# Kernel optimization log

Measured on AMD Instinct MI355X. Metric: run time of the kernel, lower is better.

Reference implementation:

```python
import jax, jax.numpy as jnp
import numpy as np

W_DIM = 512   # latent dim
CH = 512      # number of Fourier channels / output channels
SIZE = 64     # spatial size (square: size[0]=size[1])
SR = 64.0     # sampling_rate
BW = 2.0      # bandwidth
BATCH = 32


def setup_inputs() -> dict:
    key = jax.random.key(0)
    k1, k2, k3, k4, k5 = jax.random.split(key, 5)
    w = jax.random.normal(k1, (BATCH, W_DIM), jnp.float32)
    # affine FC params (weight_init=0 in original; use small random so t varies)
    affine_w = jax.random.normal(k2, (4, W_DIM), jnp.float32) * 0.1
    affine_b = jnp.array([1.0, 0.0, 0.0, 0.0], jnp.float32)
    # channel-mixing weight
    weight = jax.random.normal(k3, (CH, CH), jnp.float32)
    # freqs buffer init: randn, normalized by r*exp(r^2/4), scaled by bandwidth
    f = jax.random.normal(k4, (CH, 2), jnp.float32)
    radii = jnp.sqrt(jnp.sum(f * f, axis=1, keepdims=True))
    f = f / (radii * jnp.exp(radii * radii / 4.0)) * BW
    phases = jax.random.uniform(k5, (CH,), jnp.float32) - 0.5
    return {"w": w, "affine_w": affine_w, "affine_b": affine_b,
            "weight": weight, "freqs": f, "phases": phases}


def reference(w, affine_w, affine_b, weight, freqs, phases):
    # affine FC: FullyConnectedLayer with lr_multiplier=1 -> weight_gain = 1/sqrt(in)
    gain = np.float32(1.0 / np.sqrt(W_DIM))
    t = w @ (affine_w.T * gain) + affine_b                      # [N, 4]
    t = t / jnp.linalg.norm(t[:, :2], axis=1, keepdims=True)
    c, s, tx, ty = t[:, 0], t[:, 1], t[:, 2], t[:, 3]
    # combined transform = m_r @ m_t @ I; top-left 2x2 rotation block:
    R = jnp.stack([jnp.stack([c, -s], -1),
                   jnp.stack([s, c], -1)], axis=1)              # [N, 2, 2]
    # translation column of combined transform (m_r @ m_t)[:, :2, 2]
    trans = jnp.stack([-c * tx + s * ty, -s * tx - c * ty], -1) # [N, 2]
    ph = phases[None, :] + jnp.einsum('cd,nd->nc', freqs, trans)  # [N, C]
    fr = jnp.einsum('cd,nde->nce', freqs, R)                      # [N, C, 2]
    amp = jnp.clip(1.0 - (jnp.linalg.norm(fr, axis=2) - BW) / (SR / 2.0 - BW), 0.0, 1.0)  # [N, C]
    # affine_grid(theta, [1,1,H,W], align_corners=False): base coords (2i+1)/D - 1
    scale = np.float32(0.5 * SIZE / SR)
    xs = ((2.0 * jnp.arange(SIZE, dtype=jnp.float32) + 1.0) / SIZE - 1.0) * scale
    ys = ((2.0 * jnp.arange(SIZE, dtype=jnp.float32) + 1.0) / SIZE - 1.0) * scale
    grid = jnp.stack([jnp.broadcast_to(xs[None, :], (SIZE, SIZE)),
                      jnp.broadcast_to(ys[:, None], (SIZE, SIZE))], axis=-1)  # [H, W, 2]
    # per-pixel Fourier phase: [N, H, W, C]
    x = jnp.einsum('hwd,ncd->nhwc', grid, fr) + ph[:, None, None, :]
    x = jnp.sin(x * np.float32(2.0 * np.pi)) * amp[:, None, None, :]
    # channel projection, then to NCHW
    x = jnp.einsum('nhwc,kc->nkhw', x, weight * np.float32(1.0 / np.sqrt(CH)))
    return x  # [N, CH, H, W]
```

## Files before the change

kernel.cpp:

```cpp
#include <hip/hip_runtime.h>
#include <hip/hip_bf16.h>

#define WDIM 512
#define CHN  512
#define NB   32
#define SZ   64
#define MTOT 4096

typedef __attribute__((ext_vector_type(4))) float f32x4;
typedef __attribute__((ext_vector_type(8))) short short8;
typedef __attribute__((ext_vector_type(4))) int   int4v;
typedef __attribute__((ext_vector_type(4))) float float4v;

__global__ __launch_bounds__(512) void setup_kernel(
    const float* __restrict__ w,
    const float* __restrict__ affine_w,
    const float* __restrict__ affine_b,
    const float* __restrict__ freqs,
    const float* __restrict__ phases,
    float* __restrict__ frx_o, float* __restrict__ fry_o,
    float* __restrict__ pha_o, float* __restrict__ amp_o)
{
    const int n = blockIdx.x;
    const int tid = threadIdx.x;
    __shared__ float red[8][4];
    __shared__ float par[4];

    float wv = w[n * WDIM + tid];
    float p0 = wv * affine_w[0 * WDIM + tid];
    float p1 = wv * affine_w[1 * WDIM + tid];
    float p2 = wv * affine_w[2 * WDIM + tid];
    float p3 = wv * affine_w[3 * WDIM + tid];
    #pragma unroll
    for (int off = 32; off >= 1; off >>= 1) {
        p0 += __shfl_down(p0, off);
        p1 += __shfl_down(p1, off);
        p2 += __shfl_down(p2, off);
        p3 += __shfl_down(p3, off);
    }
    const int wave = tid >> 6;
    if ((tid & 63) == 0) {
        red[wave][0] = p0; red[wave][1] = p1;
        red[wave][2] = p2; red[wave][3] = p3;
    }
    __syncthreads();
    if (tid == 0) {
        const float gain = 0.04419417382415922f;
        float t[4];
        #pragma unroll
        for (int j = 0; j < 4; ++j) {
            float s = 0.0f;
            #pragma unroll
            for (int v = 0; v < 8; ++v) s += red[v][j];
            t[j] = s * gain + affine_b[j];
        }
        float inv = 1.0f / sqrtf(t[0] * t[0] + t[1] * t[1]);
        float c = t[0] * inv, s = t[1] * inv, tx = t[2] * inv, ty = t[3] * inv;
        par[0] = c;
        par[1] = s;
        par[2] = -c * tx + s * ty;
        par[3] = -s * tx - c * ty;
    }
    __syncthreads();
    const float c_ = par[0], s_ = par[1], tr0 = par[2], tr1 = par[3];
    const int ci = tid;
    float fx = freqs[ci * 2 + 0], fy = freqs[ci * 2 + 1];
    float frx = fx * c_ + fy * s_;
    float fry = -fx * s_ + fy * c_;
    float ph = phases[ci] + fx * tr0 + fy * tr1;
    float r = sqrtf(frx * frx + fry * fry);
    float amp = 1.0f - (r - 2.0f) * (1.0f / 30.0f);
    amp = fminf(fmaxf(amp, 0.0f), 1.0f);
    frx_o[n * CHN + ci] = frx;
    fry_o[n * CHN + ci] = fry;
    pha_o[n * CHN + ci] = ph;
    amp_o[n * CHN + ci] = amp;
}

__global__ __launch_bounds__(512) void prep_kernel(
    const float* __restrict__ frx, const float* __restrict__ amp,
    const float* __restrict__ wsrc,
    float* __restrict__ SA, float* __restrict__ CA,
    __hip_bfloat16* __restrict__ wbf)
{
    const int b = blockIdx.x;
    if (b < NB * 64) {
        const int n = b >> 6;
        const int w = b & 63;
        const int c = threadIdx.x;
        float f = frx[n * CHN + c];
        float a = amp[n * CHN + c];
        float xs = (float)(2 * w + 1) * (1.0f / 128.0f) - 0.5f;
        float arg = xs * f;
        size_t idx = ((size_t)(n * 64 + w)) * CHN + c;
        SA[idx] = a * __builtin_amdgcn_sinf(arg);
        CA[idx] = a * __builtin_amdgcn_cosf(arg);
    } else {
        int i = (b - NB * 64) * 512 + threadIdx.x;
        wbf[i] = __float2bfloat16(wsrc[i] * 0.04419417382415922f);
    }
}

__global__ __launch_bounds__(256, 2) void fused_kernel(
    const float* __restrict__ fry, const float* __restrict__ pha,
    const float* __restrict__ SA, const float* __restrict__ CA,
    const __hip_bfloat16* __restrict__ wbf,
    float* __restrict__ out)
{
    __shared__ __align__(16) __hip_bfloat16 As[128 * 64];
    __shared__ __align__(16) __hip_bfloat16 Bs[256 * 64];
    __shared__ __align__(16) float sB[2][CHN];
    __shared__ __align__(16) float cB[2][CHN];

    const int tid = threadIdx.x;
    const int mb = blockIdx.x * 128;
    const int kb = blockIdx.y * 256;
    const int n  = blockIdx.z;
    const int h0 = mb >> 6;

    #pragma unroll
    for (int u = 0; u < 2; ++u) {
        int c = tid + u * 256;
        float fy = fry[n * CHN + c];
        float ph = pha[n * CHN + c];
        #pragma unroll
        for (int hh = 0; hh < 2; ++hh) {
            float ys = (float)(2 * (h0 + hh) + 1) * (1.0f / 128.0f) - 0.5f;
            float bv = ys * fy + ph;
            sB[hh][c] = __builtin_amdgcn_sinf(bv);
            cB[hh][c] = __builtin_amdgcn_cosf(bv);
        }
    }

    const int lane = tid & 63;
    const int wid  = tid >> 6;
    const int ln15 = lane & 15;
    const int hi4  = lane >> 4;
    const int wk   = wid * 64;

    const int cc0 = (tid & 7) * 8;
    const int rb  = tid >> 3;

    const float* saL = SA + ((size_t)(n * 64 + rb)) * CHN + cc0;
    const float* saH = saL + 32 * CHN;
    const float* caL = CA + ((size_t)(n * 64 + rb)) * CHN + cc0;
    const float* caH = caL + 32 * CHN;

    f32x4 acc[4][8];
    #pragma unroll
    for (int a = 0; a < 4; ++a)
        #pragma unroll
        for (int b = 0; b < 8; ++b)
            acc[a][b] = (f32x4)0.0f;

    #pragma unroll 1
    for (int kc = 0; kc < 8; ++kc) {
        const int c0 = kc * 64;
        __syncthreads();

        #pragma unroll
        for (int u = 0; u < 8; ++u) {
            int unit = u * 256 + tid;
            int row = unit >> 3;
            int cbyte = ((unit & 7) << 4) ^ ((row & 7) << 4);
            const __hip_bfloat16* src = wbf + (size_t)(kb + row) * CHN + c0 + (cbyte >> 1);
            char* ldsbase = (char*)Bs + (u * 256 + (wid << 6)) * 16;
            __builtin_amdgcn_global_load_lds(
                (const __attribute__((address_space(1))) unsigned int*)src,
                (__attribute__((address_space(3))) unsigned int*)ldsbase, 16, 0, 0);
        }

        float4v s0 = *(const float4v*)(saL + c0), s1 = *(const float4v*)(saL + c0 + 4);
        float4v s2 = *(const float4v*)(saH + c0), s3 = *(const float4v*)(saH + c0 + 4);
        float4v q0 = *(const float4v*)(caL + c0), q1 = *(const float4v*)(caL + c0 + 4);
        float4v q2 = *(const float4v*)(caH + c0), q3 = *(const float4v*)(caH + c0 + 4);
        #pragma unroll
        for (int i = 0; i < 4; ++i) {
            int m = rb + i * 32;
            int hh = i >> 1;
            float4v A0 = (i & 1) ? s2 : s0, A1 = (i & 1) ? s3 : s1;
            float4v C0 = (i & 1) ? q2 : q0, C1 = (i & 1) ? q3 : q1;
            float4v B0 = *(const float4v*)&sB[hh][c0 + cc0];
            float4v B1 = *(const float4v*)&sB[hh][c0 + cc0 + 4];
            float4v D0 = *(const float4v*)&cB[hh][c0 + cc0];
            float4v D1 = *(const float4v*)&cB[hh][c0 + cc0 + 4];
            union { __hip_bfloat16 h[8]; int4v v; } t;
            #pragma unroll
            for (int j = 0; j < 4; ++j)
                t.h[j] = __float2bfloat16(A0[j] * D0[j] + C0[j] * B0[j]);
            #pragma unroll
            for (int j = 0; j < 4; ++j)
                t.h[4 + j] = __float2bfloat16(A1[j] * D1[j] + C1[j] * B1[j]);
            *(int4v*)((char*)As + m * 128 + ((cc0 * 2) ^ ((m & 7) << 4))) = t.v;
        }
        __syncthreads();

        #pragma unroll
        for (int kk = 0; kk < 2; ++kk) {
            short8 wf[4], ff[8];
            #pragma unroll
            for (int ki = 0; ki < 4; ++ki) {
                int row = wk + ki * 16 + ln15;
                wf[ki] = *(const short8*)((char*)Bs + row * 128 +
                          (((kk * 32 + hi4 * 8) * 2) ^ ((row & 7) << 4)));
            }
            #pragma unroll
            for (int mj = 0; mj < 8; ++mj) {
                int m = mj * 16 + ln15;
                ff[mj] = *(const short8*)((char*)As + m * 128 +
                          (((kk * 32 + hi4 * 8) * 2) ^ ((m & 7) << 4)));
            }
            #pragma unroll
            for (int ki = 0; ki < 4; ++ki)
                #pragma unroll
                for (int mj = 0; mj < 8; ++mj)
                    acc[ki][mj] = __builtin_amdgcn_mfma_f32_16x16x32_bf16(
                        wf[ki], ff[mj], acc[ki][mj], 0, 0, 0);
        }
    }

    #pragma unroll
    for (int ki = 0; ki < 4; ++ki) {
        #pragma unroll
        for (int mj = 0; mj < 8; ++mj) {
            int kg = kb + wk + ki * 16 + hi4 * 4;
            int mg = mb + mj * 16 + ln15;
            float* op = out + ((size_t)n * CHN + kg) * MTOT + mg;
            #pragma unroll
            for (int r = 0; r < 4; ++r)
                op[(size_t)r * MTOT] = acc[ki][mj][r];
        }
    }
}

extern "C" void kernel_launch(void* const* d_in, const int* in_sizes, int n_in,
                              void* d_out, int out_size, void* d_ws, size_t ws_size,
                              hipStream_t stream) {
    const float* w        = (const float*)d_in[0];
    const float* affine_w = (const float*)d_in[1];
    const float* affine_b = (const float*)d_in[2];
    const float* weight   = (const float*)d_in[3];
    const float* freqs    = (const float*)d_in[4];
    const float* phases   = (const float*)d_in[5];
    float* out = (float*)d_out;

    char* ws = (char*)d_ws;
    float* frx = (float*)(ws + 0);
    float* fry = (float*)(ws + 65536);
    float* pha = (float*)(ws + 131072);
    float* amp = (float*)(ws + 196608);
    __hip_bfloat16* wbf = (__hip_bfloat16*)(ws + 262144);
    float* SA = (float*)(ws + 786432);
    float* CA = (float*)(ws + 786432 + 4194304);

    setup_kernel<<<NB, 512, 0, stream>>>(w, affine_w, affine_b, freqs, phases,
                                         frx, fry, pha, amp);
    prep_kernel<<<NB * 64 + (CHN * CHN) / 512, 512, 0, stream>>>(
        frx, amp, weight, SA, CA, wbf);

    dim3 grid(MTOT / 128, CHN / 256, NB);
    fused_kernel<<<grid, 256, 0, stream>>>(fry, pha, SA, CA, wbf, out);
}
```

Before: 112.7 us.

## Double-buffer weight tiles and precompute row sin/cos tables in prep kernel

The fused GEMM kernel now double-buffers the bf16 weight tile in LDS. It issues the next chunk's global-to-LDS loads and A-operand loads before running MFMAs on the current chunk, using custom barriers with explicit waitcnt. The per-row sin/cos tables are moved out of the fused kernel into prep_kernel and written to global memory, so the fused kernel no longer spends time on transcendentals at its start. This adds LDS use (an extra 32KB buffer), which may limit occupancy, and adds extra global traffic for the SB/CB tables.

```diff
diff --git a/kernel.cpp b/kernel.cpp
--- a/kernel.cpp
+++ b/kernel.cpp
@@ -11,6 +11,20 @@
 typedef __attribute__((ext_vector_type(8))) short short8;
 typedef __attribute__((ext_vector_type(4))) int   int4v;
 typedef __attribute__((ext_vector_type(4))) float float4v;
+
+#define SBAR() __builtin_amdgcn_sched_barrier(0)
+__device__ __forceinline__ void bar_lgkm() {
+    SBAR();
+    asm volatile("s_waitcnt lgkmcnt(0)" ::: "memory");
+    __builtin_amdgcn_s_barrier();
+    SBAR();
+}
+__device__ __forceinline__ void bar_full() {
+    SBAR();
+    asm volatile("s_waitcnt vmcnt(0) lgkmcnt(0)" ::: "memory");
+    __builtin_amdgcn_s_barrier();
+    SBAR();
+}
 
 __global__ __launch_bounds__(512) void setup_kernel(
     const float* __restrict__ w,
@@ -78,9 +92,11 @@
 }
 
 __global__ __launch_bounds__(512) void prep_kernel(
-    const float* __restrict__ frx, const float* __restrict__ amp,
+    const float* __restrict__ frx, const float* __restrict__ fry,
+    const float* __restrict__ pha, const float* __restrict__ amp,
     const float* __restrict__ wsrc,
     float* __restrict__ SA, float* __restrict__ CA,
+    float* __restrict__ SB, float* __restrict__ CB,
     __hip_bfloat16* __restrict__ wbf)
 {
     const int b = blockIdx.x;
@@ -88,13 +104,17 @@
         const int n = b >> 6;
         const int w = b & 63;
         const int c = threadIdx.x;
-        float f = frx[n * CHN + c];
-        float a = amp[n * CHN + c];
+        float fx = frx[n * CHN + c];
+        float a  = amp[n * CHN + c];
+        float fy = fry[n * CHN + c];
+        float ph = pha[n * CHN + c];
         float xs = (float)(2 * w + 1) * (1.0f / 128.0f) - 0.5f;
-        float arg = xs * f;
         size_t idx = ((size_t)(n * 64 + w)) * CHN + c;
-        SA[idx] = a * __builtin_amdgcn_sinf(arg);
-        CA[idx] = a * __builtin_amdgcn_cosf(arg);
+        SA[idx] = a * __builtin_amdgcn_sinf(xs * fx);
+        CA[idx] = a * __builtin_amdgcn_cosf(xs * fx);
+        float bb = xs * fy + ph;
+        SB[idx] = __builtin_amdgcn_sinf(bb);
+        CB[idx] = __builtin_amdgcn_cosf(bb);
     } else {
         int i = (b - NB * 64) * 512 + threadIdx.x;
         wbf[i] = __float2bfloat16(wsrc[i] * 0.04419417382415922f);
@@ -102,15 +122,13 @@
 }
 
 __global__ __launch_bounds__(256, 2) void fused_kernel(
-    const float* __restrict__ fry, const float* __restrict__ pha,
     const float* __restrict__ SA, const float* __restrict__ CA,
+    const float* __restrict__ SB, const float* __restrict__ CB,
     const __hip_bfloat16* __restrict__ wbf,
     float* __restrict__ out)
 {
     __shared__ __align__(16) __hip_bfloat16 As[128 * 64];
-    __shared__ __align__(16) __hip_bfloat16 Bs[256 * 64];
-    __shared__ __align__(16) float sB[2][CHN];
-    __shared__ __align__(16) float cB[2][CHN];
+    __shared__ __align__(16) __hip_bfloat16 Bs[2][256 * 64];
 
     const int tid = threadIdx.x;
     const int mb = blockIdx.x * 128;
@@ -118,20 +136,6 @@
     const int n  = blockIdx.z;
     const int h0 = mb >> 6;
 
-    #pragma unroll
-    for (int u = 0; u < 2; ++u) {
-        int c = tid + u * 256;
-        float fy = fry[n * CHN + c];
-        float ph = pha[n * CHN + c];
-        #pragma unroll
-        for (int hh = 0; hh < 2; ++hh) {
-            float ys = (float)(2 * (h0 + hh) + 1) * (1.0f / 128.0f) - 0.5f;
-            float bv = ys * fy + ph;
-            sB[hh][c] = __builtin_amdgcn_sinf(bv);
-            cB[hh][c] = __builtin_amdgcn_cosf(bv);
-        }
-    }
-
     const int lane = tid & 63;
     const int wid  = tid >> 6;
     const int ln15 = lane & 15;
@@ -145,63 +149,69 @@
     const float* saH = saL + 32 * CHN;
     const float* caL = CA + ((size_t)(n * 64 + rb)) * CHN + cc0;
     const float* caH = caL + 32 * CHN;
-
-    f32x4 acc[4][8];
-    #pragma unroll
-    for (int a = 0; a < 4; ++a)
-        #pragma unroll
-        for (int b = 0; b < 8; ++b)
-            acc[a][b] = (f32x4)0.0f;
-
-    #pragma unroll 1
-    for (int kc = 0; kc < 8; ++kc) {
-        const int c0 = kc * 64;
-        __syncthreads();
-
+    const float* sb0 = SB + ((size_t)(n * 64 + h0)) * CHN + cc0;
+    const float* cb0 = CB + ((size_t)(n * 64 + h0)) * CHN + cc0;
+
+    auto stageB = [&](int buf, int c0) {
         #pragma unroll
         for (int u = 0; u < 8; ++u) {
             int unit = u * 256 + tid;
             int row = unit >> 3;
             int cbyte = ((unit & 7) << 4) ^ ((row & 7) << 4);
             const __hip_bfloat16* src = wbf + (size_t)(kb + row) * CHN + c0 + (cbyte >> 1);
-            char* ldsbase = (char*)Bs + (u * 256 + (wid << 6)) * 16;
+            char* ldsbase = (char*)Bs[buf] + (u * 256 + (wid << 6)) * 16;
             __builtin_amdgcn_global_load_lds(
                 (const __attribute__((address_space(1))) unsigned int*)src,
                 (__attribute__((address_space(3))) unsigned int*)ldsbase, 16, 0, 0);
         }
-
-        float4v s0 = *(const float4v*)(saL + c0), s1 = *(const float4v*)(saL + c0 + 4);
-        float4v s2 = *(const float4v*)(saH + c0), s3 = *(const float4v*)(saH + c0 + 4);
-        float4v q0 = *(const float4v*)(caL + c0), q1 = *(const float4v*)(caL + c0 + 4);
-        float4v q2 = *(const float4v*)(caH + c0), q3 = *(const float4v*)(caH + c0 + 4);
+    };
+
+    float4v Ps0, Ps1, Ps2, Ps3, Pq0, Pq1, Pq2, Pq3;
+    auto loadP = [&](int c0) {
+        Ps0 = *(const float4v*)(saL + c0); Ps1 = *(const float4v*)(saL + c0 + 4);
+        Ps2 = *(const float4v*)(saH + c0); Ps3 = *(const float4v*)(saH + c0 + 4);
+        Pq0 = *(const float4v*)(caL + c0); Pq1 = *(const float4v*)(caL + c0 + 4);
+        Pq2 = *(const float4v*)(caH + c0); Pq3 = *(const float4v*)(caH + c0 + 4);
+    };
+
+    auto features = [&](int c0) {
+        float4v B00 = *(const float4v*)(sb0 + c0),       B01 = *(const float4v*)(sb0 + c0 + 4);
+        float4v B10 = *(const float4v*)(sb0 + CHN + c0), B11 = *(const float4v*)(sb0 + CHN + c0 + 4);
+        float4v D00 = *(const float4v*)(cb0 + c0),       D01 = *(const float4v*)(cb0 + c0 + 4);
+        float4v D10 = *(const float4v*)(cb0 + CHN + c0), D11 = *(const float4v*)(cb0 + CHN + c0 + 4);
         #pragma unroll
         for (int i = 0; i < 4; ++i) {
             int m = rb + i * 32;
-            int hh = i >> 1;
-            float4v A0 = (i & 1) ? s2 : s0, A1 = (i & 1) ? s3 : s1;
-            float4v C0 = (i & 1) ? q2 : q0, C1 = (i & 1) ? q3 : q1;
-            float4v B0 = *(const float4v*)&sB[hh][c0 + cc0];
-            float4v B1 = *(const float4v*)&sB[hh][c0 + cc0 + 4];
-            float4v D0 = *(const float4v*)&cB[hh][c0 + cc0];
-            float4v D1 = *(const float4v*)&cB[hh][c0 + cc0 + 4];
+            float4v A0 = (i & 1) ? Ps2 : Ps0, A1 = (i & 1) ? Ps3 : Ps1;
+            float4v C0 = (i & 1) ? Pq2 : Pq0, C1 = (i & 1) ? Pq3 : Pq1;
+            float4v Sb0 = (i >> 1) ? B10 : B00, Sb1 = (i >> 1) ? B11 : B01;
+            float4v Cb0 = (i >> 1) ? D10 : D00, Cb1 = (i >> 1) ? D11 : D01;
             union { __hip_bfloat16 h[8]; int4v v; } t;
             #pragma unroll
             for (int j = 0; j < 4; ++j)
-                t.h[j] = __float2bfloat16(A0[j] * D0[j] + C0[j] * B0[j]);
+                t.h[j] = __float2bfloat16(A0[j] * Cb0[j] + C0[j] * Sb0[j]);
             #pragma unroll
             for (int j = 0; j < 4; ++j)
-                t.h[4 + j] = __float2bfloat16(A1[j] * D1[j] + C1[j] * B1[j]);
+                t.h[4 + j] = __float2bfloat16(A1[j] * Cb1[j] + C1[j] * Sb1[j]);
             *(int4v*)((char*)As + m * 128 + ((cc0 * 2) ^ ((m & 7) << 4))) = t.v;
         }
-        __syncthreads();
-
+    };
+
+    f32x4 acc[4][8];
+    #pragma unroll
+    for (int a = 0; a < 4; ++a)
+        #pragma unroll
+        for (int b = 0; b < 8; ++b)
+            acc[a][b] = (f32x4)0.0f;
+
+    auto mfmaStep = [&](int buf) {
         #pragma unroll
         for (int kk = 0; kk < 2; ++kk) {
             short8 wf[4], ff[8];
             #pragma unroll
             for (int ki = 0; ki < 4; ++ki) {
                 int row = wk + ki * 16 + ln15;
-                wf[ki] = *(const short8*)((char*)Bs + row * 128 +
+                wf[ki] = *(const short8*)((char*)Bs[buf] + row * 128 +
                           (((kk * 32 + hi4 * 8) * 2) ^ ((row & 7) << 4)));
             }
             #pragma unroll
@@ -217,7 +227,24 @@
                     acc[ki][mj] = __builtin_amdgcn_mfma_f32_16x16x32_bf16(
                         wf[ki], ff[mj], acc[ki][mj], 0, 0, 0);
         }
-    }
+    };
+
+    stageB(0, 0);
+    loadP(0);
+    features(0);
+    bar_full();
+
+    #pragma unroll 1
+    for (int kc = 0; kc < 7; ++kc) {
+        const int c0n = (kc + 1) * 64;
+        stageB((kc + 1) & 1, c0n);
+        loadP(c0n);
+        mfmaStep(kc & 1);
+        bar_lgkm();
+        features(c0n);
+        bar_full();
+    }
+    mfmaStep(1);
 
     #pragma unroll
     for (int ki = 0; ki < 4; ++ki) {
@@ -250,14 +277,16 @@
     float* pha = (float*)(ws + 131072);
     float* amp = (float*)(ws + 196608);
     __hip_bfloat16* wbf = (__hip_bfloat16*)(ws + 262144);
-    float* SA = (float*)(ws + 786432);
-    float* CA = (float*)(ws + 786432 + 4194304);
+    float* SA = (float*)(ws + (1u << 20));
+    float* CA = (float*)(ws + (1u << 20) + (4u << 20));
+    float* SB = (float*)(ws + (1u << 20) + (8u << 20));
+    float* CB = (float*)(ws + (1u << 20) + (12u << 20));
 
     setup_kernel<<<NB, 512, 0, stream>>>(w, affine_w, affine_b, freqs, phases,
                                          frx, fry, pha, amp);
     prep_kernel<<<NB * 64 + (CHN * CHN) / 512, 512, 0, stream>>>(
-        frx, amp, weight, SA, CA, wbf);
+        frx, fry, pha, amp, weight, SA, CA, SB, CB, wbf);
 
     dim3 grid(MTOT / 128, CHN / 256, NB);
-    fused_kernel<<<grid, 256, 0, stream>>>(fry, pha, SA, CA, wbf, out);
-}
+    fused_kernel<<<grid, 256, 0, stream>>>(SA, CA, SB, CB, wbf, out);
+}
```

Result: slower. 118.5 us (+5.2%).

## Fuse setup into prep, precompute row sin/cos tables, use 512-thread GEMM blocks

Applied to the files above, without the earlier changes.

Merges the setup kernel into the prep kernel. Each prep block now recomputes the affine reduction and writes per-row sin/cos tables (SB/CB) alongside the column tables, which removes one launch and the in-kernel sin/cos prologue of the GEMM. The GEMM kernel moves to 512 threads arranged as 8 waves in a 2x4 layout, each holding a 4x4 accumulator tile. This halves per-thread register use and raises the occupancy target. The cost is redundant affine reductions, repeated 64 times per batch, and extra workspace traffic for SB/CB.

```diff
diff --git a/kernel.cpp b/kernel.cpp
--- a/kernel.cpp
+++ b/kernel.cpp
@@ -12,105 +12,91 @@
 typedef __attribute__((ext_vector_type(4))) int   int4v;
 typedef __attribute__((ext_vector_type(4))) float float4v;
 
-__global__ __launch_bounds__(512) void setup_kernel(
-    const float* __restrict__ w,
+__global__ __launch_bounds__(512) void prep_kernel(
+    const float* __restrict__ win,
     const float* __restrict__ affine_w,
     const float* __restrict__ affine_b,
     const float* __restrict__ freqs,
     const float* __restrict__ phases,
-    float* __restrict__ frx_o, float* __restrict__ fry_o,
-    float* __restrict__ pha_o, float* __restrict__ amp_o)
-{
-    const int n = blockIdx.x;
-    const int tid = threadIdx.x;
-    __shared__ float red[8][4];
-    __shared__ float par[4];
-
-    float wv = w[n * WDIM + tid];
-    float p0 = wv * affine_w[0 * WDIM + tid];
-    float p1 = wv * affine_w[1 * WDIM + tid];
-    float p2 = wv * affine_w[2 * WDIM + tid];
-    float p3 = wv * affine_w[3 * WDIM + tid];
-    #pragma unroll
-    for (int off = 32; off >= 1; off >>= 1) {
-        p0 += __shfl_down(p0, off);
-        p1 += __shfl_down(p1, off);
-        p2 += __shfl_down(p2, off);
-        p3 += __shfl_down(p3, off);
-    }
-    const int wave = tid >> 6;
-    if ((tid & 63) == 0) {
-        red[wave][0] = p0; red[wave][1] = p1;
-        red[wave][2] = p2; red[wave][3] = p3;
-    }
-    __syncthreads();
-    if (tid == 0) {
-        const float gain = 0.04419417382415922f;
-        float t[4];
-        #pragma unroll
-        for (int j = 0; j < 4; ++j) {
-            float s = 0.0f;
-            #pragma unroll
-            for (int v = 0; v < 8; ++v) s += red[v][j];
-            t[j] = s * gain + affine_b[j];
-        }
-        float inv = 1.0f / sqrtf(t[0] * t[0] + t[1] * t[1]);
-        float c = t[0] * inv, s = t[1] * inv, tx = t[2] * inv, ty = t[3] * inv;
-        par[0] = c;
-        par[1] = s;
-        par[2] = -c * tx + s * ty;
-        par[3] = -s * tx - c * ty;
-    }
-    __syncthreads();
-    const float c_ = par[0], s_ = par[1], tr0 = par[2], tr1 = par[3];
-    const int ci = tid;
-    float fx = freqs[ci * 2 + 0], fy = freqs[ci * 2 + 1];
-    float frx = fx * c_ + fy * s_;
-    float fry = -fx * s_ + fy * c_;
-    float ph = phases[ci] + fx * tr0 + fy * tr1;
-    float r = sqrtf(frx * frx + fry * fry);
-    float amp = 1.0f - (r - 2.0f) * (1.0f / 30.0f);
-    amp = fminf(fmaxf(amp, 0.0f), 1.0f);
-    frx_o[n * CHN + ci] = frx;
-    fry_o[n * CHN + ci] = fry;
-    pha_o[n * CHN + ci] = ph;
-    amp_o[n * CHN + ci] = amp;
-}
-
-__global__ __launch_bounds__(512) void prep_kernel(
-    const float* __restrict__ frx, const float* __restrict__ amp,
     const float* __restrict__ wsrc,
     float* __restrict__ SA, float* __restrict__ CA,
+    float* __restrict__ SB, float* __restrict__ CB,
     __hip_bfloat16* __restrict__ wbf)
 {
     const int b = blockIdx.x;
+    const int tid = threadIdx.x;
     if (b < NB * 64) {
         const int n = b >> 6;
         const int w = b & 63;
-        const int c = threadIdx.x;
-        float f = frx[n * CHN + c];
-        float a = amp[n * CHN + c];
+        __shared__ float red[8][4];
+        __shared__ float par[4];
+
+        float wv = win[n * WDIM + tid];
+        float p0 = wv * affine_w[0 * WDIM + tid];
+        float p1 = wv * affine_w[1 * WDIM + tid];
+        float p2 = wv * affine_w[2 * WDIM + tid];
+        float p3 = wv * affine_w[3 * WDIM + tid];
+        #pragma unroll
+        for (int off = 32; off >= 1; off >>= 1) {
+            p0 += __shfl_down(p0, off);
+            p1 += __shfl_down(p1, off);
+            p2 += __shfl_down(p2, off);
+            p3 += __shfl_down(p3, off);
+        }
+        const int wave = tid >> 6;
+        if ((tid & 63) == 0) {
+            red[wave][0] = p0; red[wave][1] = p1;
+            red[wave][2] = p2; red[wave][3] = p3;
+        }
+        __syncthreads();
+        if (tid == 0) {
+            const float gain = 0.04419417382415922f;
+            float t[4];
+            #pragma unroll
+            for (int j = 0; j < 4; ++j) {
+                float s = 0.0f;
+                #pragma unroll
+                for (int v = 0; v < 8; ++v) s += red[v][j];
+                t[j] = s * gain + affine_b[j];
+            }
+            float inv = 1.0f / sqrtf(t[0] * t[0] + t[1] * t[1]);
+            float c = t[0] * inv, s = t[1] * inv, tx = t[2] * inv, ty = t[3] * inv;
+            par[0] = c;
+            par[1] = s;
+            par[2] = -c * tx + s * ty;
+            par[3] = -s * tx - c * ty;
+        }
+        __syncthreads();
+        const float c_ = par[0], s_ = par[1], tr0 = par[2], tr1 = par[3];
+        const int c = tid;
+        float fx = freqs[c * 2 + 0], fy = freqs[c * 2 + 1];
+        float frx = fx * c_ + fy * s_;
+        float fry = -fx * s_ + fy * c_;
+        float ph = phases[c] + fx * tr0 + fy * tr1;
+        float r = sqrtf(frx * frx + fry * fry);
+        float amp = 1.0f - (r - 2.0f) * (1.0f / 30.0f);
+        amp = fminf(fmaxf(amp, 0.0f), 1.0f);
         float xs = (float)(2 * w + 1) * (1.0f / 128.0f) - 0.5f;
-        float arg = xs * f;
         size_t idx = ((size_t)(n * 64 + w)) * CHN + c;
-        SA[idx] = a * __builtin_amdgcn_sinf(arg);
-        CA[idx] = a * __builtin_amdgcn_cosf(arg);
+        SA[idx] = amp * __builtin_amdgcn_sinf(xs * frx);
+        CA[idx] = amp * __builtin_amdgcn_cosf(xs * frx);
+        float bb = xs * fry + ph;
+        SB[idx] = __builtin_amdgcn_sinf(bb);
+        CB[idx] = __builtin_amdgcn_cosf(bb);
     } else {
-        int i = (b - NB * 64) * 512 + threadIdx.x;
+        int i = (b - NB * 64) * 512 + tid;
         wbf[i] = __float2bfloat16(wsrc[i] * 0.04419417382415922f);
     }
 }
 
-__global__ __launch_bounds__(256, 2) void fused_kernel(
-    const float* __restrict__ fry, const float* __restrict__ pha,
+__global__ __launch_bounds__(512, 4) void fused_kernel(
     const float* __restrict__ SA, const float* __restrict__ CA,
+    const float* __restrict__ SB, const float* __restrict__ CB,
     const __hip_bfloat16* __restrict__ wbf,
     float* __restrict__ out)
 {
     __shared__ __align__(16) __hip_bfloat16 As[128 * 64];
     __shared__ __align__(16) __hip_bfloat16 Bs[256 * 64];
-    __shared__ __align__(16) float sB[2][CHN];
-    __shared__ __align__(16) float cB[2][CHN];
 
     const int tid = threadIdx.x;
     const int mb = blockIdx.x * 128;
@@ -118,39 +104,26 @@
     const int n  = blockIdx.z;
     const int h0 = mb >> 6;
 
-    #pragma unroll
-    for (int u = 0; u < 2; ++u) {
-        int c = tid + u * 256;
-        float fy = fry[n * CHN + c];
-        float ph = pha[n * CHN + c];
-        #pragma unroll
-        for (int hh = 0; hh < 2; ++hh) {
-            float ys = (float)(2 * (h0 + hh) + 1) * (1.0f / 128.0f) - 0.5f;
-            float bv = ys * fy + ph;
-            sB[hh][c] = __builtin_amdgcn_sinf(bv);
-            cB[hh][c] = __builtin_amdgcn_cosf(bv);
-        }
-    }
-
     const int lane = tid & 63;
     const int wid  = tid >> 6;
     const int ln15 = lane & 15;
     const int hi4  = lane >> 4;
-    const int wk   = wid * 64;
+    const int wm   = (wid >> 2) * 64;
+    const int wk   = (wid & 3) * 64;
 
     const int cc0 = (tid & 7) * 8;
     const int rb  = tid >> 3;
 
-    const float* saL = SA + ((size_t)(n * 64 + rb)) * CHN + cc0;
-    const float* saH = saL + 32 * CHN;
-    const float* caL = CA + ((size_t)(n * 64 + rb)) * CHN + cc0;
-    const float* caH = caL + 32 * CHN;
-
-    f32x4 acc[4][8];
+    const float* pSA = SA + ((size_t)(n * 64 + rb)) * CHN + cc0;
+    const float* pCA = CA + ((size_t)(n * 64 + rb)) * CHN + cc0;
+    const float* pSB = SB + ((size_t)(n * 64 + h0)) * CHN + cc0;
+    const float* pCB = CB + ((size_t)(n * 64 + h0)) * CHN + cc0;
+
+    f32x4 acc[4][4];
     #pragma unroll
     for (int a = 0; a < 4; ++a)
         #pragma unroll
-        for (int b = 0; b < 8; ++b)
+        for (int b = 0; b < 4; ++b)
             acc[a][b] = (f32x4)0.0f;
 
     #pragma unroll 1
@@ -159,61 +132,58 @@
         __syncthreads();
 
         #pragma unroll
-        for (int u = 0; u < 8; ++u) {
-            int unit = u * 256 + tid;
+        for (int u = 0; u < 4; ++u) {
+            int unit = u * 512 + tid;
             int row = unit >> 3;
             int cbyte = ((unit & 7) << 4) ^ ((row & 7) << 4);
             const __hip_bfloat16* src = wbf + (size_t)(kb + row) * CHN + c0 + (cbyte >> 1);
-            char* ldsbase = (char*)Bs + (u * 256 + (wid << 6)) * 16;
+            char* ldsbase = (char*)Bs + (u * 512 + (wid << 6)) * 16;
             __builtin_amdgcn_global_load_lds(
                 (const __attribute__((address_space(1))) unsigned int*)src,
                 (__attribute__((address_space(3))) unsigned int*)ldsbase, 16, 0, 0);
         }
 
-        float4v s0 = *(const float4v*)(saL + c0), s1 = *(const float4v*)(saL + c0 + 4);
-        float4v s2 = *(const float4v*)(saH + c0), s3 = *(const float4v*)(saH + c0 + 4);
-        float4v q0 = *(const float4v*)(caL + c0), q1 = *(const float4v*)(caL + c0 + 4);
-        float4v q2 = *(const float4v*)(caH + c0), q3 = *(const float4v*)(caH + c0 + 4);
-        #pragma unroll
-        for (int i = 0; i < 4; ++i) {
-            int m = rb + i * 32;
-            int hh = i >> 1;
-            float4v A0 = (i & 1) ? s2 : s0, A1 = (i & 1) ? s3 : s1;
-            float4v C0 = (i & 1) ? q2 : q0, C1 = (i & 1) ? q3 : q1;
-            float4v B0 = *(const float4v*)&sB[hh][c0 + cc0];
-            float4v B1 = *(const float4v*)&sB[hh][c0 + cc0 + 4];
-            float4v D0 = *(const float4v*)&cB[hh][c0 + cc0];
-            float4v D1 = *(const float4v*)&cB[hh][c0 + cc0 + 4];
-            union { __hip_bfloat16 h[8]; int4v v; } t;
-            #pragma unroll
-            for (int j = 0; j < 4; ++j)
-                t.h[j] = __float2bfloat16(A0[j] * D0[j] + C0[j] * B0[j]);
-            #pragma unroll
-            for (int j = 0; j < 4; ++j)
-                t.h[4 + j] = __float2bfloat16(A1[j] * D1[j] + C1[j] * B1[j]);
-            *(int4v*)((char*)As + m * 128 + ((cc0 * 2) ^ ((m & 7) << 4))) = t.v;
+        {
+            float4v P0 = *(const float4v*)(pSA + c0), P1 = *(const float4v*)(pSA + c0 + 4);
+            float4v Q0 = *(const float4v*)(pCA + c0), Q1 = *(const float4v*)(pCA + c0 + 4);
+            #pragma unroll
+            for (int i = 0; i < 2; ++i) {
+                int m = rb + i * 64;
+                float4v Sb0 = *(const float4v*)(pSB + i * CHN + c0);
+                float4v Sb1 = *(const float4v*)(pSB + i * CHN + c0 + 4);
+                float4v Cb0 = *(const float4v*)(pCB + i * CHN + c0);
+                float4v Cb1 = *(const float4v*)(pCB + i * CHN + c0 + 4);
+                union { __hip_bfloat16 h[8]; int4v v; } t;
+                #pragma unroll
+                for (int j = 0; j < 4; ++j)
+                    t.h[j] = __float2bfloat16(P0[j] * Cb0[j] + Q0[j] * Sb0[j]);
+                #pragma unroll
+                for (int j = 0; j < 4; ++j)
+                    t.h[4 + j] = __float2bfloat16(P1[j] * Cb1[j] + Q1[j] * Sb1[j]);
+                *(int4v*)((char*)As + m * 128 + ((cc0 * 2) ^ ((m & 7) << 4))) = t.v;
+            }
         }
         __syncthreads();
 
         #pragma unroll
         for (int kk = 0; kk < 2; ++kk) {
-            short8 wf[4], ff[8];
+            short8 wf[4], ff[4];
             #pragma unroll
             for (int ki = 0; ki < 4; ++ki) {
                 int row = wk + ki * 16 + ln15;
                 wf[ki] = *(const short8*)((char*)Bs + row * 128 +
-                          (((kk * 32 + hi4 * 8) * 2) ^ ((row & 7) << 4)));
-            }
-            #pragma unroll
-            for (int mj = 0; mj < 8; ++mj) {
-                int m = mj * 16 + ln15;
+                          ((kk * 64 + hi4 * 16) ^ ((row & 7) << 4)));
+            }
+            #pragma unroll
+            for (int mj = 0; mj < 4; ++mj) {
+                int m = wm + mj * 16 + ln15;
                 ff[mj] = *(const short8*)((char*)As + m * 128 +
-                          (((kk * 32 + hi4 * 8) * 2) ^ ((m & 7) << 4)));
+                          ((kk * 64 + hi4 * 16) ^ ((m & 7) << 4)));
             }
             #pragma unroll
             for (int ki = 0; ki < 4; ++ki)
                 #pragma unroll
-                for (int mj = 0; mj < 8; ++mj)
+                for (int mj = 0; mj < 4; ++mj)
                     acc[ki][mj] = __builtin_amdgcn_mfma_f32_16x16x32_bf16(
                         wf[ki], ff[mj], acc[ki][mj], 0, 0, 0);
         }
@@ -222,9 +192,9 @@
     #pragma unroll
     for (int ki = 0; ki < 4; ++ki) {
         #pragma unroll
-        for (int mj = 0; mj < 8; ++mj) {
+        for (int mj = 0; mj < 4; ++mj) {
             int kg = kb + wk + ki * 16 + hi4 * 4;
-            int mg = mb + mj * 16 + ln15;
+            int mg = mb + wm + mj * 16 + ln15;
             float* op = out + ((size_t)n * CHN + kg) * MTOT + mg;
             #pragma unroll
             for (int r = 0; r < 4; ++r)
@@ -245,19 +215,15 @@
     float* out = (float*)d_out;
 
     char* ws = (char*)d_ws;
-    float* frx = (float*)(ws + 0);
-    float* fry = (float*)(ws + 65536);
-    float* pha = (float*)(ws + 131072);
-    float* amp = (float*)(ws + 196608);
-    __hip_bfloat16* wbf = (__hip_bfloat16*)(ws + 262144);
-    float* SA = (float*)(ws + 786432);
-    float* CA = (float*)(ws + 786432 + 4194304);
-
-    setup_kernel<<<NB, 512, 0, stream>>>(w, affine_w, affine_b, freqs, phases,
-                                         frx, fry, pha, amp);
+    __hip_bfloat16* wbf = (__hip_bfloat16*)(ws);
+    float* SA = (float*)(ws + (1u << 20));
+    float* CA = (float*)(ws + (1u << 20) + (4u << 20));
+    float* SB = (float*)(ws + (1u << 20) + (8u << 20));
+    float* CB = (float*)(ws + (1u << 20) + (12u << 20));
+
     prep_kernel<<<NB * 64 + (CHN * CHN) / 512, 512, 0, stream>>>(
-        frx, amp, weight, SA, CA, wbf);
+        w, affine_w, affine_b, freqs, phases, weight, SA, CA, SB, CB, wbf);
 
     dim3 grid(MTOT / 128, CHN / 256, NB);
-    fused_kernel<<<grid, 256, 0, stream>>>(fry, pha, SA, CA, wbf, out);
+    fused_kernel<<<grid, 512, 0, stream>>>(SA, CA, SB, CB, wbf, out);
 }
```

New measurement: 148.1 us. 1.31x slower.
